# Kernel tuning notes

Hardware: AMD Instinct MI355X
Metric: run time of the kernel (lower is better)

Reference implementation:

```python
import jax, jax.numpy as jnp
import numpy as np

B, L, E, H = 8, 1024, 1024, 16
A = E // H  # head dim 64
SCALE = A ** -0.5
NEG = jnp.finfo(jnp.float32).min


def setup_inputs() -> dict:
    key = jax.random.key(0)
    k1, k2, k3, k4, k5 = jax.random.split(key, 5)
    embeddings = jax.random.normal(k1, (B, L, E), dtype=jnp.float32)
    attn_mask = jax.random.randint(k2, (B, H, L, L), 0, 2) == 1
    attn_bias = jax.random.normal(k3, (B, H, L, L), dtype=jnp.float32)
    W_qkv = jax.random.normal(k4, (3 * E, E), dtype=jnp.float32) * (E ** -0.5)
    W_out = jax.random.normal(k5, (E, E), dtype=jnp.float32) * (E ** -0.5)
    return {"embeddings": embeddings, "attn_mask": attn_mask,
            "attn_bias": attn_bias, "W_qkv": W_qkv, "W_out": W_out}


def reference(embeddings, attn_mask, attn_bias, W_qkv, W_out):
    # fused QKV projection: torch Linear -> x @ W.T
    qkv = embeddings @ W_qkv.T                      # [B, L, 3E]
    qkv = qkv.reshape(B, L, H, 3 * A).transpose(0, 2, 1, 3)  # [B, H, L, 3A]
    q, k, v = jnp.split(qkv, 3, axis=-1)            # each [B, H, L, A]
    attn = jnp.einsum('bhqa,bhka->bhqk', q, k) * SCALE
    attn = attn + attn_bias
    attn = jnp.where(attn_mask, NEG, attn)
    attn = jax.nn.softmax(attn, axis=-1)
    values = jnp.einsum('bhqk,bhka->bhqa', attn, v)  # [B, H, L, A]
    values = values.transpose(0, 2, 1, 3).reshape(B, L, E)
    return values @ W_out.T
```

## Files before the change

### kernel.cpp

```cpp
#include <hip/hip_runtime.h>
#include <cstdint>
#include <cstddef>


typedef __bf16 bf16;
typedef __attribute__((ext_vector_type(8))) __bf16 bf16x8;
typedef __attribute__((ext_vector_type(4))) float f32x4;

#define MFMA_BF16(a, b, c) __builtin_amdgcn_mfma_f32_16x16x32_bf16(a, b, c, 0, 0, 0)

static constexpr float SCALE_ = 0.125f;
static constexpr float NEGF  = -3.4028234663852886e38f;

__device__ __forceinline__ void gload_lds16(const bf16* g, bf16* l) {
  __builtin_amdgcn_global_load_lds((const __attribute__((address_space(1))) void*)g,
                                   (__attribute__((address_space(3))) void*)l,
                                   16, 0, 0);
}

__device__ __forceinline__ bf16x8 cvt8(const float* p) {
  f32x4 a = *(const f32x4*)p;
  f32x4 b = *(const f32x4*)(p + 4);
  bf16x8 r = {(bf16)a[0], (bf16)a[1], (bf16)a[2], (bf16)a[3],
              (bf16)b[0], (bf16)b[1], (bf16)b[2], (bf16)b[3]};
  return r;
}

__global__ __launch_bounds__(256) void k_qkv(const float* __restrict__ X,
                                             const float* __restrict__ W,
                                             bf16* __restrict__ Q,
                                             bf16* __restrict__ Kc,
                                             bf16* __restrict__ Vt) {
  constexpr int K = 1024;
  __shared__ __align__(16) bf16 As[128 * 64];
  __shared__ __align__(16) bf16 Bs[128 * 64];
  const int t = threadIdx.x;
  const int lane = t & 63, w = t >> 6;
  const int wr = w >> 1, wc = w & 1;
  const int li = lane & 15, g = lane >> 4;
  const int m0 = (blockIdx.x & 63) * 128;
  const int n0 = (blockIdx.x >> 6) * 128;

  f32x4 acc[4][4] = {};

  for (int kt = 0; kt < K; kt += 64) {
#pragma unroll
    for (int it = 0; it < 4; ++it) {
      int c = it * 256 + t;
      int row = c >> 3, col = (c & 7) << 3;
      *(bf16x8*)(As + c * 8) = cvt8(X + (size_t)(m0 + row) * K + kt + col);
      *(bf16x8*)(Bs + c * 8) = cvt8(W + (size_t)(n0 + row) * K + kt + col);
    }
    __syncthreads();
#pragma unroll
    for (int kk = 0; kk < 2; ++kk) {
      bf16x8 af[4], bfr[4];
#pragma unroll
      for (int i = 0; i < 4; ++i)
        af[i] = *(const bf16x8*)(As + (wr * 64 + i * 16 + li) * 64 + kk * 32 + g * 8);
#pragma unroll
      for (int j = 0; j < 4; ++j)
        bfr[j] = *(const bf16x8*)(Bs + (wc * 64 + j * 16 + li) * 64 + kk * 32 + g * 8);
#pragma unroll
      for (int i = 0; i < 4; ++i)
#pragma unroll
        for (int j = 0; j < 4; ++j)
          acc[i][j] = MFMA_BF16(af[i], bfr[j], acc[i][j]);
    }
    __syncthreads();
  }

#pragma unroll
  for (int i = 0; i < 4; ++i) {
#pragma unroll
    for (int j = 0; j < 4; ++j) {
      int col = n0 + wc * 64 + j * 16 + li;
      int h = col / 192, r = col % 192;
#pragma unroll
      for (int rg = 0; rg < 4; ++rg) {
        int row = m0 + wr * 64 + i * 16 + g * 4 + rg;
        int b = row >> 10, l = row & 1023;
        bf16 v = (bf16)acc[i][j][rg];
        if (r < 64)
          Q[((size_t)((b * 16 + h) * 1024 + l)) * 64 + r] = v;
        else if (r < 128)
          Kc[((size_t)((b * 16 + h) * 1024 + l)) * 64 + (r - 64)] = v;
        else
          Vt[((size_t)((b * 16 + h) * 64 + (r - 128))) * 1024 + l] = v;
      }
    }
  }
}

__global__ __launch_bounds__(256) void k_attn(const bf16* __restrict__ Q,
                                              const bf16* __restrict__ Kc,
                                              const bf16* __restrict__ Vt,
                                              const float* __restrict__ bias,
                                              const int* __restrict__ mask,
                                              bf16* __restrict__ Vals) {
  __shared__ __align__(16) bf16 Plds[4][16][72];
  const int t = threadIdx.x, lane = t & 63, w = t >> 6;
  const int li = lane & 15, g = lane >> 4;
  const int bh = blockIdx.y;
  const int b = bh >> 4, h = bh & 15;
  const int q0 = blockIdx.x * 64 + w * 16;

  const bf16* Qbase = Q + ((size_t)bh << 10) * 64;
  const bf16* Kbase = Kc + ((size_t)bh << 10) * 64;
  const bf16* Vbase = Vt + ((size_t)bh << 6) * 1024;
  const size_t bm0 = ((size_t)bh << 20);

  bf16x8 qf[2];
#pragma unroll
  for (int c = 0; c < 2; ++c)
    qf[c] = *(const bf16x8*)(Qbase + (size_t)(q0 + li) * 64 + c * 32 + g * 8);

  f32x4 oacc[4] = {};
  float mrun[4] = {NEGF, NEGF, NEGF, NEGF};
  float lrun[4] = {0.f, 0.f, 0.f, 0.f};

  for (int kkt = 0; kkt < 1024; kkt += 64) {
    f32x4 s[4];
#pragma unroll
    for (int kkf = 0; kkf < 4; ++kkf) {
      f32x4 ss = {0.f, 0.f, 0.f, 0.f};
#pragma unroll
      for (int c = 0; c < 2; ++c) {
        bf16x8 kf = *(const bf16x8*)(Kbase + (size_t)(kkt + kkf * 16 + li) * 64 + c * 32 + g * 8);
        ss = MFMA_BF16(qf[c], kf, ss);
      }
      s[kkf] = ss;
    }
    float tmax[4] = {NEGF, NEGF, NEGF, NEGF};
#pragma unroll
    for (int kkf = 0; kkf < 4; ++kkf) {
#pragma unroll
      for (int rg = 0; rg < 4; ++rg) {
        size_t idx = bm0 + (size_t)(q0 + g * 4 + rg) * 1024 + kkt + kkf * 16 + li;
        float sv = s[kkf][rg] * SCALE_ + bias[idx];
        sv = mask[idx] ? NEGF : sv;
        s[kkf][rg] = sv;
        tmax[rg] = fmaxf(tmax[rg], sv);
      }
    }
#pragma unroll
    for (int rg = 0; rg < 4; ++rg) {
      float v = tmax[rg];
#pragma unroll
      for (int d = 1; d < 16; d <<= 1) v = fmaxf(v, __shfl_xor(v, d));
      tmax[rg] = v;
    }
    float mnew[4], corr[4], psum[4];
#pragma unroll
    for (int rg = 0; rg < 4; ++rg) {
      mnew[rg] = fmaxf(mrun[rg], tmax[rg]);
      corr[rg] = __expf(mrun[rg] - mnew[rg]);
      psum[rg] = 0.f;
    }
#pragma unroll
    for (int kkf = 0; kkf < 4; ++kkf) {
#pragma unroll
      for (int rg = 0; rg < 4; ++rg) {
        float p = __expf(s[kkf][rg] - mnew[rg]);
        psum[rg] += p;
        Plds[w][g * 4 + rg][kkf * 16 + li] = (bf16)p;
      }
    }
#pragma unroll
    for (int rg = 0; rg < 4; ++rg) {
      float v = psum[rg];
#pragma unroll
      for (int d = 1; d < 16; d <<= 1) v += __shfl_xor(v, d);
      lrun[rg] = lrun[rg] * corr[rg] + v;
      mrun[rg] = mnew[rg];
    }
#pragma unroll
    for (int af = 0; af < 4; ++af)
#pragma unroll
      for (int rg = 0; rg < 4; ++rg) oacc[af][rg] *= corr[rg];
    __syncthreads();
#pragma unroll
    for (int c = 0; c < 2; ++c) {
      bf16x8 pf = *(const bf16x8*)(&Plds[w][li][c * 32 + g * 8]);
#pragma unroll
      for (int af = 0; af < 4; ++af) {
        bf16x8 vf = *(const bf16x8*)(Vbase + (size_t)(af * 16 + li) * 1024 + kkt + c * 32 + g * 8);
        oacc[af] = MFMA_BF16(pf, vf, oacc[af]);
      }
    }
    __syncthreads();
  }

#pragma unroll
  for (int af = 0; af < 4; ++af) {
#pragma unroll
    for (int rg = 0; rg < 4; ++rg) {
      int q = q0 + g * 4 + rg;
      int col = h * 64 + af * 16 + li;
      Vals[(((size_t)(b * 1024 + q)) << 10) + col] = (bf16)(oacc[af][rg] / lrun[rg]);
    }
  }
}

__global__ __launch_bounds__(256) void k_out(const bf16* __restrict__ X,
                                             const float* __restrict__ W,
                                             float* __restrict__ Out) {
  constexpr int K = 1024;
  __shared__ __align__(16) bf16 As[128 * 64];
  __shared__ __align__(16) bf16 Bs[128 * 64];
  const int t = threadIdx.x;
  const int lane = t & 63, w = t >> 6;
  const int wr = w >> 1, wc = w & 1;
  const int li = lane & 15, g = lane >> 4;
  const int m0 = (blockIdx.x & 63) * 128;
  const int n0 = (blockIdx.x >> 6) * 128;

  f32x4 acc[4][4] = {};

  for (int kt = 0; kt < K; kt += 64) {
#pragma unroll
    for (int it = 0; it < 4; ++it) {
      int c = it * 256 + t;
      int row = c >> 3, col = (c & 7) << 3;
      gload_lds16(X + (size_t)(m0 + row) * K + kt + col, As + c * 8);
      *(bf16x8*)(Bs + c * 8) = cvt8(W + (size_t)(n0 + row) * K + kt + col);
    }
    __syncthreads();
#pragma unroll
    for (int kk = 0; kk < 2; ++kk) {
      bf16x8 af[4], bfr[4];
#pragma unroll
      for (int i = 0; i < 4; ++i)
        af[i] = *(const bf16x8*)(As + (wr * 64 + i * 16 + li) * 64 + kk * 32 + g * 8);
#pragma unroll
      for (int j = 0; j < 4; ++j)
        bfr[j] = *(const bf16x8*)(Bs + (wc * 64 + j * 16 + li) * 64 + kk * 32 + g * 8);
#pragma unroll
      for (int i = 0; i < 4; ++i)
#pragma unroll
        for (int j = 0; j < 4; ++j)
          acc[i][j] = MFMA_BF16(af[i], bfr[j], acc[i][j]);
    }
    __syncthreads();
  }

#pragma unroll
  for (int i = 0; i < 4; ++i) {
#pragma unroll
    for (int j = 0; j < 4; ++j) {
      int col = n0 + wc * 64 + j * 16 + li;
#pragma unroll
      for (int rg = 0; rg < 4; ++rg) {
        int row = m0 + wr * 64 + i * 16 + g * 4 + rg;
        Out[((size_t)row << 10) + col] = acc[i][j][rg];
      }
    }
  }
}

extern "C" void kernel_launch(void* const* d_in, const int* in_sizes, int n_in,
                              void* d_out, int out_size, void* d_ws, size_t ws_size,
                              hipStream_t stream) {
  const float* emb  = (const float*)d_in[0];
  const int*   mask = (const int*)d_in[1];
  const float* bias = (const float*)d_in[2];
  const float* Wqkv = (const float*)d_in[3];
  const float* Wout = (const float*)d_in[4];
  float* out = (float*)d_out;

  const size_t HEADS_ELEMS = (size_t)8 * 16 * 1024 * 64;
  bf16* Q    = (bf16*)d_ws;
  bf16* Kc   = Q + HEADS_ELEMS;
  bf16* Vt   = Kc + HEADS_ELEMS;
  bf16* Vals = Vt + HEADS_ELEMS;

  k_qkv<<<dim3(64 * 24), 256, 0, stream>>>(emb, Wqkv, Q, Kc, Vt);
  k_attn<<<dim3(16, 128), 256, 0, stream>>>(Q, Kc, Vt, bias, mask, Vals);
  k_out<<<dim3(64 * 8), 256, 0, stream>>>(Vals, Wout, out);
}
```

Baseline: 505.9 us.

## Transpose QK MFMA so each lane owns a query row; vectorize bias/mask loads

Swaps the MFMA operands for S so each lane holds four consecutive key columns of one query row. Bias and mask can then be read as 16-byte vectors per row instead of scattered scalar loads. Row max and sum reductions shrink to two cross-lane shuffles, and P is written to LDS in 4-wide packed stores. The block-wide __syncthreads pair is replaced by a per-wave lgkmcnt wait with a double-buffered P tile, and the grid is flattened so neighbouring blocks cover different heads. The risks are the extra shuffles to redistribute the correction and normalisation factors, and reliance on wave-local LDS ordering.

```diff
diff --git a/kernel.cpp b/kernel.cpp
--- a/kernel.cpp
+++ b/kernel.cpp
@@ -5,7 +5,9 @@
 
 typedef __bf16 bf16;
 typedef __attribute__((ext_vector_type(8))) __bf16 bf16x8;
+typedef __attribute__((ext_vector_type(4))) __bf16 bf16x4;
 typedef __attribute__((ext_vector_type(4))) float f32x4;
+typedef __attribute__((ext_vector_type(4))) int i32x4;
 
 #define MFMA_BF16(a, b, c) __builtin_amdgcn_mfma_f32_16x16x32_bf16(a, b, c, 0, 0, 0)
 
@@ -98,17 +100,20 @@
                                               const float* __restrict__ bias,
                                               const int* __restrict__ mask,
                                               bf16* __restrict__ Vals) {
-  __shared__ __align__(16) bf16 Plds[4][16][72];
+  __shared__ __align__(16) bf16 Plds[4][2][16][80];
   const int t = threadIdx.x, lane = t & 63, w = t >> 6;
   const int li = lane & 15, g = lane >> 4;
-  const int bh = blockIdx.y;
+  const int lid = blockIdx.x;
+  const int bh = lid & 127;
+  const int qt = lid >> 7;
   const int b = bh >> 4, h = bh & 15;
-  const int q0 = blockIdx.x * 64 + w * 16;
+  const int q0 = qt * 64 + w * 16;
 
   const bf16* Qbase = Q + ((size_t)bh << 10) * 64;
   const bf16* Kbase = Kc + ((size_t)bh << 10) * 64;
   const bf16* Vbase = Vt + ((size_t)bh << 6) * 1024;
-  const size_t bm0 = ((size_t)bh << 20);
+  const float* brow = bias + ((size_t)bh << 20) + (size_t)(q0 + li) * 1024 + g * 4;
+  const int*   mrow = mask + ((size_t)bh << 20) + (size_t)(q0 + li) * 1024 + g * 4;
 
   bf16x8 qf[2];
 #pragma unroll
@@ -116,10 +121,21 @@
     qf[c] = *(const bf16x8*)(Qbase + (size_t)(q0 + li) * 64 + c * 32 + g * 8);
 
   f32x4 oacc[4] = {};
-  float mrun[4] = {NEGF, NEGF, NEGF, NEGF};
-  float lrun[4] = {0.f, 0.f, 0.f, 0.f};
-
-  for (int kkt = 0; kkt < 1024; kkt += 64) {
+  float mrun = NEGF;
+  float lrun = 0.f;
+
+  for (int kt6 = 0; kt6 < 16; ++kt6) {
+    const int kkt = kt6 * 64;
+    const int par = kt6 & 1;
+
+    f32x4 b4[4];
+    i32x4 m4[4];
+#pragma unroll
+    for (int kkf = 0; kkf < 4; ++kkf) {
+      b4[kkf] = *(const f32x4*)(brow + kkt + kkf * 16);
+      m4[kkf] = *(const i32x4*)(mrow + kkt + kkf * 16);
+    }
+
     f32x4 s[4];
 #pragma unroll
     for (int kkf = 0; kkf < 4; ++kkf) {
@@ -127,77 +143,76 @@
 #pragma unroll
       for (int c = 0; c < 2; ++c) {
         bf16x8 kf = *(const bf16x8*)(Kbase + (size_t)(kkt + kkf * 16 + li) * 64 + c * 32 + g * 8);
-        ss = MFMA_BF16(qf[c], kf, ss);
+        ss = MFMA_BF16(kf, qf[c], ss);
       }
       s[kkf] = ss;
     }
-    float tmax[4] = {NEGF, NEGF, NEGF, NEGF};
+
+    float tmax = NEGF;
 #pragma unroll
     for (int kkf = 0; kkf < 4; ++kkf) {
 #pragma unroll
       for (int rg = 0; rg < 4; ++rg) {
-        size_t idx = bm0 + (size_t)(q0 + g * 4 + rg) * 1024 + kkt + kkf * 16 + li;
-        float sv = s[kkf][rg] * SCALE_ + bias[idx];
-        sv = mask[idx] ? NEGF : sv;
+        float sv = s[kkf][rg] * SCALE_ + b4[kkf][rg];
+        sv = m4[kkf][rg] ? NEGF : sv;
         s[kkf][rg] = sv;
-        tmax[rg] = fmaxf(tmax[rg], sv);
-      }
-    }
-#pragma unroll
-    for (int rg = 0; rg < 4; ++rg) {
-      float v = tmax[rg];
-#pragma unroll
-      for (int d = 1; d < 16; d <<= 1) v = fmaxf(v, __shfl_xor(v, d));
-      tmax[rg] = v;
-    }
-    float mnew[4], corr[4], psum[4];
-#pragma unroll
-    for (int rg = 0; rg < 4; ++rg) {
-      mnew[rg] = fmaxf(mrun[rg], tmax[rg]);
-      corr[rg] = __expf(mrun[rg] - mnew[rg]);
-      psum[rg] = 0.f;
-    }
-#pragma unroll
-    for (int kkf = 0; kkf < 4; ++kkf) {
-#pragma unroll
-      for (int rg = 0; rg < 4; ++rg) {
-        float p = __expf(s[kkf][rg] - mnew[rg]);
-        psum[rg] += p;
-        Plds[w][g * 4 + rg][kkf * 16 + li] = (bf16)p;
-      }
-    }
-#pragma unroll
-    for (int rg = 0; rg < 4; ++rg) {
-      float v = psum[rg];
-#pragma unroll
-      for (int d = 1; d < 16; d <<= 1) v += __shfl_xor(v, d);
-      lrun[rg] = lrun[rg] * corr[rg] + v;
-      mrun[rg] = mnew[rg];
-    }
+        tmax = fmaxf(tmax, sv);
+      }
+    }
+    tmax = fmaxf(tmax, __shfl_xor(tmax, 16));
+    tmax = fmaxf(tmax, __shfl_xor(tmax, 32));
+
+    float mnew = fmaxf(mrun, tmax);
+    float corr = __expf(mrun - mnew);
+    float psum = 0.f;
+
+#pragma unroll
+    for (int kkf = 0; kkf < 4; ++kkf) {
+      float p0 = __expf(s[kkf][0] - mnew);
+      float p1 = __expf(s[kkf][1] - mnew);
+      float p2 = __expf(s[kkf][2] - mnew);
+      float p3 = __expf(s[kkf][3] - mnew);
+      psum += (p0 + p1) + (p2 + p3);
+      bf16x4 pk = {(bf16)p0, (bf16)p1, (bf16)p2, (bf16)p3};
+      *(bf16x4*)(&Plds[w][par][li][kkf * 16 + g * 4]) = pk;
+    }
+    psum += __shfl_xor(psum, 16);
+    psum += __shfl_xor(psum, 32);
+    lrun = lrun * corr + psum;
+    mrun = mnew;
+
+    float cq[4];
+#pragma unroll
+    for (int rg = 0; rg < 4; ++rg) cq[rg] = __shfl(corr, g * 4 + rg);
 #pragma unroll
     for (int af = 0; af < 4; ++af)
 #pragma unroll
-      for (int rg = 0; rg < 4; ++rg) oacc[af][rg] *= corr[rg];
-    __syncthreads();
+      for (int rg = 0; rg < 4; ++rg) oacc[af][rg] *= cq[rg];
+
+    asm volatile("s_waitcnt lgkmcnt(0)" ::: "memory");
+    __builtin_amdgcn_sched_barrier(0);
+
 #pragma unroll
     for (int c = 0; c < 2; ++c) {
-      bf16x8 pf = *(const bf16x8*)(&Plds[w][li][c * 32 + g * 8]);
+      bf16x8 pf = *(const bf16x8*)(&Plds[w][par][li][c * 32 + g * 8]);
 #pragma unroll
       for (int af = 0; af < 4; ++af) {
         bf16x8 vf = *(const bf16x8*)(Vbase + (size_t)(af * 16 + li) * 1024 + kkt + c * 32 + g * 8);
         oacc[af] = MFMA_BF16(pf, vf, oacc[af]);
       }
     }
-    __syncthreads();
-  }
-
+  }
+
+  float linv[4];
+#pragma unroll
+  for (int rg = 0; rg < 4; ++rg) linv[rg] = 1.0f / __shfl(lrun, g * 4 + rg);
 #pragma unroll
   for (int af = 0; af < 4; ++af) {
 #pragma unroll
     for (int rg = 0; rg < 4; ++rg) {
       int q = q0 + g * 4 + rg;
       int col = h * 64 + af * 16 + li;
-      Vals[(((size_t)(b * 1024 + q)) << 10) + col] = (bf16)(oacc[af][rg] / lrun[rg]);
+      Vals[(((size_t)(b * 1024 + q)) << 10) + col] = (bf16)(oacc[af][rg] * linv[rg]);
     }
   }
 }
@@ -275,6 +290,6 @@
   bf16* Vals = Vt + HEADS_ELEMS;
 
   k_qkv<<<dim3(64 * 24), 256, 0, stream>>>(emb, Wqkv, Q, Kc, Vt);
-  k_attn<<<dim3(16, 128), 256, 0, stream>>>(Q, Kc, Vt, bias, mask, Vals);
+  k_attn<<<dim3(2048), 256, 0, stream>>>(Q, Kc, Vt, bias, mask, Vals);
   k_out<<<dim3(64 * 8), 256, 0, stream>>>(Vals, Wout, out);
 }
```

Result: slower. 553.8 us (+9.5%).
